# Optimization experiments

Measured on AMD Instinct MI355X. Metric: run time of the kernel, lower is better.

The kernel has to match this reference:

```python
import jax, jax.numpy as jnp
import numpy as np

B, T, DM, H, D = 2, 2048, 1024, 16, 64
SCALE = D ** -0.5


def setup_inputs() -> dict:
    key = jax.random.key(0)
    ks = jax.random.split(key, 7)
    std = DM ** -0.5
    inp = {
        "x": jax.random.normal(ks[0], (B, T, DM), dtype=jnp.float32),
        "Wq_re": jax.random.normal(ks[1], (DM, H * D), dtype=jnp.float32) * std,
        "Wq_im": jax.random.normal(ks[2], (DM, H * D), dtype=jnp.float32) * std,
        "Wk_re": jax.random.normal(ks[3], (DM, H * D), dtype=jnp.float32) * std,
        "Wk_im": jax.random.normal(ks[4], (DM, H * D), dtype=jnp.float32) * std,
        "Wv": jax.random.normal(ks[5], (DM, H * D), dtype=jnp.float32) * std,
        "Wo": jax.random.normal(ks[6], (H * D, DM), dtype=jnp.float32) * std,
    }
    # standard RoPE angle cache: theta[t, d] = t * 10000^(-d/D)
    inv_freq = 1.0 / (10000.0 ** (np.arange(D, dtype=np.float32) / D))
    ang = np.arange(T, dtype=np.float32)[:, None] * inv_freq[None, :]
    inp["cos"] = jnp.asarray(np.cos(ang))
    inp["sin"] = jnp.asarray(np.sin(ang))
    return inp


def _split(x, W):
    # [B,T,DM] @ [DM,H*D] -> [B,H,T,D]
    return (x @ W).reshape(B, T, H, D).transpose(0, 2, 1, 3)


def reference(x, Wq_re, Wq_im, Wk_re, Wk_im, Wv, Wo, cos, sin):
    q_re, q_im = _split(x, Wq_re), _split(x, Wq_im)
    k_re, k_im = _split(x, Wk_re), _split(x, Wk_im)

    # complex RoPE: rotate (re, im) by e^{i*theta}; cos/sin broadcast over b,h
    c = cos[None, None]  # [1,1,T,D]
    s = sin[None, None]
    q_re, q_im = q_re * c - q_im * s, q_re * s + q_im * c
    k_re, k_im = k_re * c - k_im * s, k_re * s + k_im * c

    # Hermitian inner product real part: q_re.k_re + q_im.k_im
    scores = (jnp.einsum("bhqd,bhkd->bhqk", q_re, k_re)
              + jnp.einsum("bhqd,bhkd->bhqk", q_im, k_im)) * SCALE

    causal = jnp.tril(jnp.ones((T, T), dtype=bool))
    scores = jnp.where(causal[None, None], scores, -jnp.inf)
    weights = jax.nn.softmax(scores, axis=-1)

    v = _split(x, Wv)
    out = jnp.einsum("bhqk,bhkd->bhqd", weights, v)  # [B,H,T,D]
    out = out.transpose(0, 2, 1, 3).reshape(B, T, H * D)
    return out @ Wo
```

## Files before the change

kernel.cpp:

```cpp
#include <hip/hip_runtime.h>
#include <math.h>

#define SCALE_ 0.125f

typedef _Float16 half_t;
typedef __attribute__((ext_vector_type(8))) _Float16 f16x8;
typedef __attribute__((ext_vector_type(4))) _Float16 f16x4;
typedef __attribute__((ext_vector_type(4))) float f32x4;

#define AS1 __attribute__((address_space(1)))
#define AS3 __attribute__((address_space(3)))

__device__ __forceinline__ f32x4 mfma16(f16x8 a, f16x8 b, f32x4 c) {
  return __builtin_amdgcn_mfma_f32_16x16x32_f16(a, b, c, 0, 0, 0);
}
__device__ __forceinline__ void gload16(const void* g, void* l) {
  __builtin_amdgcn_global_load_lds((const AS1 void*)g, (AS3 void*)l, 16, 0, 0);
}
__device__ __forceinline__ void split2(float f, half_t* h, half_t* l) {
  half_t hh = (half_t)f;
  *h = hh;
  *l = (half_t)(f - (float)hh);
}

__global__ __launch_bounds__(256) void convw_kernel(
    const float* __restrict__ W0, const float* __restrict__ W1,
    const float* __restrict__ W2, const float* __restrict__ W3,
    const float* __restrict__ W4, const float* __restrict__ W5,
    half_t* __restrict__ wh, half_t* __restrict__ wl)
{
  const int z = blockIdx.z;
  const float* W = (z == 0) ? W0 : (z == 1) ? W1 : (z == 2) ? W2
                  : (z == 3) ? W3 : (z == 4) ? W4 : W5;
  half_t* outh = wh + z * 1048576;
  half_t* outl = wl + z * 1048576;
  const int n0 = blockIdx.x * 32, k0 = blockIdx.y * 32;
  const int t = threadIdx.x, r = t >> 3, c4 = (t & 7) * 4;
  __shared__ float lds[32][33];
  float4 v = *(const float4*)&W[(k0 + r) * 1024 + n0 + c4];
  lds[r][c4 + 0] = v.x; lds[r][c4 + 1] = v.y;
  lds[r][c4 + 2] = v.z; lds[r][c4 + 3] = v.w;
  __syncthreads();
  f16x4 oh, ol;
#pragma unroll
  for (int j = 0; j < 4; ++j) {
    const float f = lds[c4 + j][r];
    half_t hv, lv; split2(f, &hv, &lv);
    oh[j] = hv; ol[j] = lv;
  }
  *(f16x4*)&outh[(n0 + r) * 1024 + k0 + c4] = oh;
  *(f16x4*)&outl[(n0 + r) * 1024 + k0 + c4] = ol;
}

__global__ __launch_bounds__(256) void convx_kernel(
    const float* __restrict__ x, half_t* __restrict__ xh, half_t* __restrict__ xl)
{
  const int i = (blockIdx.x * 256 + threadIdx.x) * 4;
  float4 v = *(const float4*)&x[i];
  float vv[4] = {v.x, v.y, v.z, v.w};
  f16x4 oh, ol;
#pragma unroll
  for (int j = 0; j < 4; ++j) {
    half_t hv, lv; split2(vv[j], &hv, &lv);
    oh[j] = hv; ol[j] = lv;
  }
  *(f16x4*)&xh[i] = oh;
  *(f16x4*)&xl[i] = ol;
}

__global__ __launch_bounds__(256) void gemm_kernel(
    const half_t* __restrict__ Agh, const half_t* __restrict__ Agl,
    const half_t* __restrict__ wh, const half_t* __restrict__ wl,
    half_t* __restrict__ qth, half_t* __restrict__ qtl,
    half_t* __restrict__ kth, half_t* __restrict__ ktl,
    half_t* __restrict__ vTh, half_t* __restrict__ vTl,
    float* __restrict__ outp, int final_mode)
{
  __shared__ half_t Ash[4096], Asl[4096], Bsh[4096], Bsl[4096];
  const int z = blockIdx.z;
  const int widx = final_mode ? 5 : z;
  const half_t* Bth = wh + widx * 1048576;
  const half_t* Btl = wl + widx * 1048576;

  const int n0 = blockIdx.x * 128, m0 = blockIdx.y * 128;
  const int tid = threadIdx.x, lane = tid & 63, wid = tid >> 6;
  const int wr = wid >> 1, wc = wid & 1, l15 = lane & 15, l4 = lane >> 4;

  f32x4 acc[4][4];
#pragma unroll
  for (int i = 0; i < 4; ++i)
#pragma unroll
    for (int j = 0; j < 4; ++j) acc[i][j] = (f32x4){0.f, 0.f, 0.f, 0.f};

  const int s0 = wid * 64 + lane, s1 = s0 + 256;
  const int r0 = s0 >> 2, c0 = (s0 & 3) * 8;
  const int r1 = s1 >> 2, c1 = (s1 & 3) * 8;
  half_t* Ah0 = Ash + wid * 512;        half_t* Ah1 = Ash + 2048 + wid * 512;
  half_t* Al0 = Asl + wid * 512;        half_t* Al1 = Asl + 2048 + wid * 512;
  half_t* Bh0 = Bsh + wid * 512;        half_t* Bh1 = Bsh + 2048 + wid * 512;
  half_t* Bl0 = Bsl + wid * 512;        half_t* Bl1 = Bsl + 2048 + wid * 512;

  for (int k0 = 0; k0 < 1024; k0 += 32) {
    __syncthreads();
    gload16(Agh + (m0 + r0) * 1024 + k0 + c0, Ah0);
    gload16(Agh + (m0 + r1) * 1024 + k0 + c1, Ah1);
    gload16(Agl + (m0 + r0) * 1024 + k0 + c0, Al0);
    gload16(Agl + (m0 + r1) * 1024 + k0 + c1, Al1);
    gload16(Bth + (n0 + r0) * 1024 + k0 + c0, Bh0);
    gload16(Bth + (n0 + r1) * 1024 + k0 + c1, Bh1);
    gload16(Btl + (n0 + r0) * 1024 + k0 + c0, Bl0);
    gload16(Btl + (n0 + r1) * 1024 + k0 + c1, Bl1);
    __syncthreads();
    f16x8 ah[4], al[4], bh[4], bl[4];
#pragma unroll
    for (int i = 0; i < 4; ++i) {
      const int ro = (wr * 64 + i * 16 + l15) * 32 + l4 * 8;
      ah[i] = *(const f16x8*)&Ash[ro];
      al[i] = *(const f16x8*)&Asl[ro];
    }
#pragma unroll
    for (int j = 0; j < 4; ++j) {
      const int ro = (wc * 64 + j * 16 + l15) * 32 + l4 * 8;
      bh[j] = *(const f16x8*)&Bsh[ro];
      bl[j] = *(const f16x8*)&Bsl[ro];
    }
#pragma unroll
    for (int i = 0; i < 4; ++i)
#pragma unroll
      for (int j = 0; j < 4; ++j) {
        acc[i][j] = mfma16(ah[i], bh[j], acc[i][j]);
        acc[i][j] = mfma16(ah[i], bl[j], acc[i][j]);
        acc[i][j] = mfma16(al[i], bh[j], acc[i][j]);
      }
  }

#pragma unroll
  for (int i = 0; i < 4; ++i) {
    const int mb = m0 + wr * 64 + i * 16 + l4 * 4;
#pragma unroll
    for (int j = 0; j < 4; ++j) {
      const int n = n0 + wc * 64 + j * 16 + l15;
      if (final_mode) {
#pragma unroll
        for (int r = 0; r < 4; ++r) outp[(mb + r) * 1024 + n] = acc[i][j][r];
      } else if (z < 4) {
        half_t* dh = (z < 2) ? qth : kth;
        half_t* dl = (z < 2) ? qtl : ktl;
        const int colr = (n >> 6) * 128 + (n & 63) + ((z & 1) ? 64 : 0);
#pragma unroll
        for (int r = 0; r < 4; ++r) {
          half_t hv, lv; split2(acc[i][j][r], &hv, &lv);
          dh[(mb + r) * 2048 + colr] = hv;
          dl[(mb + r) * 2048 + colr] = lv;
        }
      } else {
        const int hh = n >> 6, d = n & 63;
        const int bq = mb >> 11, t = mb & 2047;
        f16x4 vh4, vl4;
#pragma unroll
        for (int r = 0; r < 4; ++r) {
          half_t hv, lv; split2(acc[i][j][r], &hv, &lv);
          vh4[r] = hv; vl4[r] = lv;
        }
        const int off = ((bq * 16 + hh) * 64 + d) * 2048 + t;
        *(f16x4*)&vTh[off] = vh4;
        *(f16x4*)&vTl[off] = vl4;
      }
    }
  }
}

__global__ __launch_bounds__(256) void rope_kernel(
    const half_t* __restrict__ qth, const half_t* __restrict__ qtl,
    const half_t* __restrict__ kth, const half_t* __restrict__ ktl,
    const float* __restrict__ cosb, const float* __restrict__ sinb,
    half_t* __restrict__ qbh, half_t* __restrict__ qbl,
    half_t* __restrict__ kbh, half_t* __restrict__ kbl)
{
  const int z = blockIdx.y;
  const int g = blockIdx.x * 4 + (threadIdx.x >> 6);
  const int d = threadIdx.x & 63;
  const int m = g >> 4, h = g & 15;
  const int b = m >> 11, t = m & 2047;
  const half_t* sh = (z ? kth : qth) + m * 2048 + h * 128;
  const half_t* sl = (z ? ktl : qtl) + m * 2048 + h * 128;
  const float re = (float)sh[d] + (float)sl[d];
  const float im = (float)sh[64 + d] + (float)sl[64 + d];
  const float c = cosb[t * 64 + d], s = sinb[t * 64 + d];
  float rer = re * c - im * s;
  float imr = re * s + im * c;
  if (z == 0) { rer *= SCALE_; imr *= SCALE_; }
  half_t* dh = (z ? kbh : qbh) + ((b * 16 + h) * 2048 + t) * 128;
  half_t* dl = (z ? kbl : qbl) + ((b * 16 + h) * 2048 + t) * 128;
  half_t hv, lv;
  split2(rer, &hv, &lv); dh[d] = hv;      dl[d] = lv;
  split2(imr, &hv, &lv); dh[64 + d] = hv; dl[64 + d] = lv;
}

__global__ __launch_bounds__(256) void attn_kernel(
    const half_t* __restrict__ qbh, const half_t* __restrict__ qbl,
    const half_t* __restrict__ kbh, const half_t* __restrict__ kbl,
    const half_t* __restrict__ vTh, const half_t* __restrict__ vTl,
    half_t* __restrict__ abh, half_t* __restrict__ abl)
{
  const int qt = (int)gridDim.x - 1 - (int)blockIdx.x;
  const int bh = blockIdx.y;
  const int b = bh >> 4, h = bh & 15;
  const int tid = threadIdx.x, lane = tid & 63, w = tid >> 6;
  const int l15 = lane & 15, l4 = lane >> 4;
  const int q0 = qt * 64;

  __shared__ half_t Kh[8192], Kl[8192];
  __shared__ half_t Vh[4096], Vl[4096];
  __shared__ half_t Ph[4096], Pl[4096];

  f16x8 qh[4], ql[4];
  {
    const int qoff = (bh * 2048 + q0 + w * 16 + l15) * 128;
#pragma unroll
    for (int c = 0; c < 4; ++c) {
      qh[c] = *(const f16x8*)(qbh + qoff + c * 32 + l4 * 8);
      ql[c] = *(const f16x8*)(qbl + qoff + c * 32 + l4 * 8);
    }
  }

  f32x4 o[4];
#pragma unroll
  for (int n = 0; n < 4; ++n) o[n] = (f32x4){0.f, 0.f, 0.f, 0.f};
  float mrow[4] = {-3e38f, -3e38f, -3e38f, -3e38f};
  float lrow[4] = {0.f, 0.f, 0.f, 0.f};

  const half_t* kh_p = kbh + bh * 2048 * 128;
  const half_t* kl_p = kbl + bh * 2048 * 128;
  const half_t* vh_p = vTh + bh * 64 * 2048;
  const half_t* vl_p = vTl + bh * 64 * 2048;

  for (int kt = 0; kt <= qt; ++kt) {
    const int k0 = kt * 64;
    __syncthreads();
    {
      f16x8 kh_[4], kl_[4], vh_[2], vl_[2];
#pragma unroll
      for (int it = 0; it < 4; ++it) {
        const int sIdx = it * 256 + tid, row = sIdx >> 4, slot = sIdx & 15;
        kh_[it] = *(const f16x8*)(kh_p + (k0 + row) * 128 + slot * 8);
        kl_[it] = *(const f16x8*)(kl_p + (k0 + row) * 128 + slot * 8);
      }
#pragma unroll
      for (int it = 0; it < 2; ++it) {
        const int sIdx = it * 256 + tid, row = sIdx >> 3, slot = sIdx & 7;
        vh_[it] = *(const f16x8*)(vh_p + row * 2048 + k0 + slot * 8);
        vl_[it] = *(const f16x8*)(vl_p + row * 2048 + k0 + slot * 8);
      }
#pragma unroll
      for (int it = 0; it < 4; ++it) {
        const int sIdx = it * 256 + tid, row = sIdx >> 4, slot = sIdx & 15;
        const int sp = (slot & 8) | ((slot & 7) ^ (row & 7));
        *(f16x8*)&Kh[row * 128 + sp * 8] = kh_[it];
        *(f16x8*)&Kl[row * 128 + sp * 8] = kl_[it];
      }
#pragma unroll
      for (int it = 0; it < 2; ++it) {
        const int sIdx = it * 256 + tid, row = sIdx >> 3, slot = sIdx & 7;
        const int sp = slot ^ (row & 7);
        *(f16x8*)&Vh[row * 64 + sp * 8] = vh_[it];
        *(f16x8*)&Vl[row * 64 + sp * 8] = vl_[it];
      }
    }
    __syncthreads();

    f32x4 s[4];
#pragma unroll
    for (int n = 0; n < 4; ++n) s[n] = (f32x4){0.f, 0.f, 0.f, 0.f};
#pragma unroll
    for (int c = 0; c < 4; ++c) {
#pragma unroll
      for (int n = 0; n < 4; ++n) {
        const int row = n * 16 + l15;
        const int slot = c * 4 + l4;
        const int sp = (slot & 8) | ((slot & 7) ^ (row & 7));
        const f16x8 kfh = *(const f16x8*)&Kh[row * 128 + sp * 8];
        const f16x8 kfl = *(const f16x8*)&Kl[row * 128 + sp * 8];
        s[n] = mfma16(qh[c], kfh, s[n]);
        s[n] = mfma16(qh[c], kfl, s[n]);
        s[n] = mfma16(ql[c], kfh, s[n]);
      }
    }

    if (kt == qt) {
#pragma unroll
      for (int n = 0; n < 4; ++n)
#pragma unroll
        for (int r = 0; r < 4; ++r)
          if (n * 16 + l15 > w * 16 + l4 * 4 + r) s[n][r] = -3e38f;
    }

#pragma unroll
    for (int r = 0; r < 4; ++r) {
      float mx = fmaxf(fmaxf(s[0][r], s[1][r]), fmaxf(s[2][r], s[3][r]));
      mx = fmaxf(mx, __shfl_xor(mx, 1));
      mx = fmaxf(mx, __shfl_xor(mx, 2));
      mx = fmaxf(mx, __shfl_xor(mx, 4));
      mx = fmaxf(mx, __shfl_xor(mx, 8));
      const float mnew = fmaxf(mrow[r], mx);
      const float alpha = __expf(mrow[r] - mnew);
      float p[4];
#pragma unroll
      for (int n = 0; n < 4; ++n) p[n] = __expf(s[n][r] - mnew);
      float rs = p[0] + p[1] + p[2] + p[3];
      rs += __shfl_xor(rs, 1);
      rs += __shfl_xor(rs, 2);
      rs += __shfl_xor(rs, 4);
      rs += __shfl_xor(rs, 8);
      lrow[r] = lrow[r] * alpha + rs;
      mrow[r] = mnew;
#pragma unroll
      for (int n = 0; n < 4; ++n) o[n][r] *= alpha;
      const int prow = w * 16 + l4 * 4 + r;
#pragma unroll
      for (int n = 0; n < 4; ++n) {
        const int col = n * 16 + l15;
        const int sp = (col >> 3) ^ (prow & 7);
        half_t hv, lv; split2(p[n], &hv, &lv);
        Ph[prow * 64 + sp * 8 + (col & 7)] = hv;
        Pl[prow * 64 + sp * 8 + (col & 7)] = lv;
      }
    }
    __syncthreads();

#pragma unroll
    for (int c = 0; c < 2; ++c) {
      const int prow = w * 16 + l15;
      const int sp = (c * 4 + l4) ^ (prow & 7);
      const f16x8 pfh = *(const f16x8*)&Ph[prow * 64 + sp * 8];
      const f16x8 pfl = *(const f16x8*)&Pl[prow * 64 + sp * 8];
#pragma unroll
      for (int n = 0; n < 4; ++n) {
        const int vrow = n * 16 + l15;
        const int sp2 = (c * 4 + l4) ^ (vrow & 7);
        const f16x8 vfh = *(const f16x8*)&Vh[vrow * 64 + sp2 * 8];
        const f16x8 vfl = *(const f16x8*)&Vl[vrow * 64 + sp2 * 8];
        o[n] = mfma16(pfh, vfh, o[n]);
        o[n] = mfma16(pfh, vfl, o[n]);
        o[n] = mfma16(pfl, vfh, o[n]);
      }
    }
  }

  const int mg = b * 2048 + q0 + w * 16 + l4 * 4;
#pragma unroll
  for (int r = 0; r < 4; ++r) {
    const float inv = 1.0f / lrow[r];
    const int m = mg + r;
#pragma unroll
    for (int n = 0; n < 4; ++n) {
      half_t hv, lv; split2(o[n][r] * inv, &hv, &lv);
      abh[m * 1024 + h * 64 + n * 16 + l15] = hv;
      abl[m * 1024 + h * 64 + n * 16 + l15] = lv;
    }
  }
}

extern "C" void kernel_launch(void* const* d_in, const int* in_sizes, int n_in,
                              void* d_out, int out_size, void* d_ws,
                              size_t ws_size, hipStream_t stream) {
  const float* x    = (const float*)d_in[0];
  const float* Wqre = (const float*)d_in[1];
  const float* Wqim = (const float*)d_in[2];
  const float* Wkre = (const float*)d_in[3];
  const float* Wkim = (const float*)d_in[4];
  const float* Wv   = (const float*)d_in[5];
  const float* Wo   = (const float*)d_in[6];
  const float* cosb = (const float*)d_in[7];
  const float* sinb = (const float*)d_in[8];

  char* w = (char*)d_ws;
  const size_t MB = (size_t)1 << 20;
  half_t* wh6 = (half_t*)(w + 0 * MB);
  half_t* wl6 = (half_t*)(w + 12 * MB);
  half_t* xh  = (half_t*)(w + 24 * MB);
  half_t* xl  = (half_t*)(w + 32 * MB);
  half_t* qth = (half_t*)(w + 40 * MB);
  half_t* qtl = (half_t*)(w + 56 * MB);
  half_t* kth = (half_t*)(w + 72 * MB);
  half_t* ktl = (half_t*)(w + 88 * MB);
  half_t* qbh = (half_t*)(w + 104 * MB);
  half_t* qbl = (half_t*)(w + 120 * MB);
  half_t* kbh = (half_t*)(w + 136 * MB);
  half_t* kbl = (half_t*)(w + 152 * MB);
  half_t* vTh = (half_t*)(w + 168 * MB);
  half_t* vTl = (half_t*)(w + 176 * MB);
  half_t* abh = (half_t*)(w + 40 * MB);
  half_t* abl = (half_t*)(w + 48 * MB);

  dim3 blk(256);
  convw_kernel<<<dim3(32, 32, 6), blk, 0, stream>>>(Wqre, Wqim, Wkre, Wkim, Wv,
                                                    Wo, wh6, wl6);
  convx_kernel<<<dim3(4096), blk, 0, stream>>>(x, xh, xl);
  gemm_kernel<<<dim3(8, 32, 5), blk, 0, stream>>>(xh, xl, wh6, wl6, qth, qtl,
                                                  kth, ktl, vTh, vTl, nullptr, 0);
  rope_kernel<<<dim3(16384, 2), blk, 0, stream>>>(qth, qtl, kth, ktl, cosb,
                                                  sinb, qbh, qbl, kbh, kbl);
  attn_kernel<<<dim3(32, 32), blk, 0, stream>>>(qbh, qbl, kbh, kbl, vTh, vTl,
                                                abh, abl);
  gemm_kernel<<<dim3(8, 32, 1), blk, 0, stream>>>(abh, abl, wh6, wl6, nullptr,
                                                  nullptr, nullptr, nullptr,
                                                  nullptr, nullptr,
                                                  (float*)d_out, 1);
}
```

Before: 565.9 us.

## Restructure attention kernel: 512-thread blocks, 32-key double-buffered async LDS loads

The attention kernel now uses 512 threads (8 waves) per block covering 128 query rows, with 32-key tiles. K/V tiles are loaded with global_load_lds into double-buffered shared memory so the next tile's load overlaps compute. Waves whose queries lie entirely before a tile skip its compute, and the P tile is written and read within a wave without a block barrier. This aims to hide global latency and cut register-staged copies and barriers, at the cost of smaller MFMA tiles per iteration and more loop iterations.

Result: no change. 570.6 us (+0.8%).

```diff
diff --git a/kernel.cpp b/kernel.cpp
--- a/kernel.cpp
+++ b/kernel.cpp
@@ -197,7 +197,7 @@
   split2(imr, &hv, &lv); dh[64 + d] = hv; dl[64 + d] = lv;
 }
 
-__global__ __launch_bounds__(256) void attn_kernel(
+__global__ __launch_bounds__(512) void attn_kernel(
     const half_t* __restrict__ qbh, const half_t* __restrict__ qbl,
     const half_t* __restrict__ kbh, const half_t* __restrict__ kbl,
     const half_t* __restrict__ vTh, const half_t* __restrict__ vTl,
@@ -208,10 +208,10 @@
   const int b = bh >> 4, h = bh & 15;
   const int tid = threadIdx.x, lane = tid & 63, w = tid >> 6;
   const int l15 = lane & 15, l4 = lane >> 4;
-  const int q0 = qt * 64;
-
-  __shared__ half_t Kh[8192], Kl[8192];
-  __shared__ half_t Vh[4096], Vl[4096];
+  const int q0 = qt * 128;
+
+  __shared__ half_t Kh[2][4096], Kl[2][4096];
+  __shared__ half_t Vh[2][2048], Vl[2][2048];
   __shared__ half_t Ph[4096], Pl[4096];
 
   f16x8 qh[4], ql[4];
@@ -230,84 +230,81 @@
   float mrow[4] = {-3e38f, -3e38f, -3e38f, -3e38f};
   float lrow[4] = {0.f, 0.f, 0.f, 0.f};
 
-  const half_t* kh_p = kbh + bh * 2048 * 128;
-  const half_t* kl_p = kbl + bh * 2048 * 128;
-  const half_t* vh_p = vTh + bh * 64 * 2048;
-  const half_t* vl_p = vTl + bh * 64 * 2048;
-
-  for (int kt = 0; kt <= qt; ++kt) {
-    const int k0 = kt * 64;
+  const half_t* kh_p = kbh + (size_t)bh * 2048 * 128;
+  const half_t* kl_p = kbl + (size_t)bh * 2048 * 128;
+  const half_t* vh_p = vTh + (size_t)bh * 64 * 2048;
+  const half_t* vl_p = vTl + (size_t)bh * 64 * 2048;
+
+  const int krow = w * 4 + (lane >> 4);
+  const int ks = lane & 15;
+  const int kg = (ks & 8) | ((ks & 7) ^ (krow & 7));
+  const int vrow = (w & 3) * 16 + (lane >> 2);
+  const int vs = lane & 3;
+  const int vg = vs ^ ((vrow >> 1) & 3);
+  const bool vhi = (w < 4);
+
+  const int nkt = 4 * (qt + 1);
+  const int qminw = q0 + w * 16, qmaxw = qminw + 15;
+
+  gload16(kh_p + (krow) * 128 + kg * 8, &Kh[0][w * 512]);
+  gload16(kl_p + (krow) * 128 + kg * 8, &Kl[0][w * 512]);
+  if (vhi) gload16(vh_p + vrow * 2048 + vg * 8, &Vh[0][(w & 3) * 512]);
+  else     gload16(vl_p + vrow * 2048 + vg * 8, &Vl[0][(w & 3) * 512]);
+
+  for (int kt = 0; kt < nkt; ++kt) {
+    const int k0 = kt * 32;
+    const int cb = kt & 1;
     __syncthreads();
+
     {
-      f16x8 kh_[4], kl_[4], vh_[2], vl_[2];
-#pragma unroll
-      for (int it = 0; it < 4; ++it) {
-        const int sIdx = it * 256 + tid, row = sIdx >> 4, slot = sIdx & 15;
-        kh_[it] = *(const f16x8*)(kh_p + (k0 + row) * 128 + slot * 8);
-        kl_[it] = *(const f16x8*)(kl_p + (k0 + row) * 128 + slot * 8);
-      }
-#pragma unroll
-      for (int it = 0; it < 2; ++it) {
-        const int sIdx = it * 256 + tid, row = sIdx >> 3, slot = sIdx & 7;
-        vh_[it] = *(const f16x8*)(vh_p + row * 2048 + k0 + slot * 8);
-        vl_[it] = *(const f16x8*)(vl_p + row * 2048 + k0 + slot * 8);
-      }
-#pragma unroll
-      for (int it = 0; it < 4; ++it) {
-        const int sIdx = it * 256 + tid, row = sIdx >> 4, slot = sIdx & 15;
-        const int sp = (slot & 8) | ((slot & 7) ^ (row & 7));
-        *(f16x8*)&Kh[row * 128 + sp * 8] = kh_[it];
-        *(f16x8*)&Kl[row * 128 + sp * 8] = kl_[it];
-      }
-#pragma unroll
-      for (int it = 0; it < 2; ++it) {
-        const int sIdx = it * 256 + tid, row = sIdx >> 3, slot = sIdx & 7;
-        const int sp = slot ^ (row & 7);
-        *(f16x8*)&Vh[row * 64 + sp * 8] = vh_[it];
-        *(f16x8*)&Vl[row * 64 + sp * 8] = vl_[it];
-      }
-    }
-    __syncthreads();
-
-    f32x4 s[4];
-#pragma unroll
-    for (int n = 0; n < 4; ++n) s[n] = (f32x4){0.f, 0.f, 0.f, 0.f};
+      const int k0n = (kt + 1 < nkt) ? k0 + 32 : 0;
+      const int nb = cb ^ 1;
+      gload16(kh_p + (k0n + krow) * 128 + kg * 8, &Kh[nb][w * 512]);
+      gload16(kl_p + (k0n + krow) * 128 + kg * 8, &Kl[nb][w * 512]);
+      if (vhi) gload16(vh_p + vrow * 2048 + k0n + vg * 8, &Vh[nb][(w & 3) * 512]);
+      else     gload16(vl_p + vrow * 2048 + k0n + vg * 8, &Vl[nb][(w & 3) * 512]);
+    }
+
+    if (k0 > qmaxw) continue;
+
+    f32x4 s[2];
+    s[0] = (f32x4){0.f, 0.f, 0.f, 0.f};
+    s[1] = (f32x4){0.f, 0.f, 0.f, 0.f};
 #pragma unroll
     for (int c = 0; c < 4; ++c) {
 #pragma unroll
-      for (int n = 0; n < 4; ++n) {
+      for (int n = 0; n < 2; ++n) {
         const int row = n * 16 + l15;
-        const int slot = c * 4 + l4;
-        const int sp = (slot & 8) | ((slot & 7) ^ (row & 7));
-        const f16x8 kfh = *(const f16x8*)&Kh[row * 128 + sp * 8];
-        const f16x8 kfl = *(const f16x8*)&Kl[row * 128 + sp * 8];
+        const int co = c * 4 + l4;
+        const int sr = (co & 8) | ((co & 7) ^ (row & 7));
+        const f16x8 kfh = *(const f16x8*)&Kh[cb][row * 128 + sr * 8];
+        const f16x8 kfl = *(const f16x8*)&Kl[cb][row * 128 + sr * 8];
         s[n] = mfma16(qh[c], kfh, s[n]);
         s[n] = mfma16(qh[c], kfl, s[n]);
         s[n] = mfma16(ql[c], kfh, s[n]);
       }
     }
 
-    if (kt == qt) {
-#pragma unroll
-      for (int n = 0; n < 4; ++n)
+    if (k0 + 31 > qminw) {
+#pragma unroll
+      for (int n = 0; n < 2; ++n)
 #pragma unroll
         for (int r = 0; r < 4; ++r)
-          if (n * 16 + l15 > w * 16 + l4 * 4 + r) s[n][r] = -3e38f;
+          if (k0 + n * 16 + l15 > qminw + l4 * 4 + r) s[n][r] = -3e38f;
     }
 
 #pragma unroll
     for (int r = 0; r < 4; ++r) {
-      float mx = fmaxf(fmaxf(s[0][r], s[1][r]), fmaxf(s[2][r], s[3][r]));
+      float mx = fmaxf(s[0][r], s[1][r]);
       mx = fmaxf(mx, __shfl_xor(mx, 1));
       mx = fmaxf(mx, __shfl_xor(mx, 2));
       mx = fmaxf(mx, __shfl_xor(mx, 4));
       mx = fmaxf(mx, __shfl_xor(mx, 8));
       const float mnew = fmaxf(mrow[r], mx);
       const float alpha = __expf(mrow[r] - mnew);
-      float p[4];
-#pragma unroll
-      for (int n = 0; n < 4; ++n) p[n] = __expf(s[n][r] - mnew);
-      float rs = p[0] + p[1] + p[2] + p[3];
+      const float p0 = __expf(s[0][r] - mnew);
+      const float p1 = __expf(s[1][r] - mnew);
+      float rs = p0 + p1;
       rs += __shfl_xor(rs, 1);
       rs += __shfl_xor(rs, 2);
       rs += __shfl_xor(rs, 4);
@@ -317,29 +314,33 @@
 #pragma unroll
       for (int n = 0; n < 4; ++n) o[n][r] *= alpha;
       const int prow = w * 16 + l4 * 4 + r;
+      const int psw = (prow >> 2) & 3;
+      half_t hv, lv;
+      split2(p0, &hv, &lv);
+      {
+        const int col = l15, sp = (col >> 3) ^ psw;
+        Ph[prow * 32 + sp * 8 + (col & 7)] = hv;
+        Pl[prow * 32 + sp * 8 + (col & 7)] = lv;
+      }
+      split2(p1, &hv, &lv);
+      {
+        const int col = 16 + l15, sp = (col >> 3) ^ psw;
+        Ph[prow * 32 + sp * 8 + (col & 7)] = hv;
+        Pl[prow * 32 + sp * 8 + (col & 7)] = lv;
+      }
+    }
+
+    {
+      const int prow = w * 16 + l15;
+      const int spp = l4 ^ ((prow >> 2) & 3);
+      const f16x8 pfh = *(const f16x8*)&Ph[prow * 32 + spp * 8];
+      const f16x8 pfl = *(const f16x8*)&Pl[prow * 32 + spp * 8];
 #pragma unroll
       for (int n = 0; n < 4; ++n) {
-        const int col = n * 16 + l15;
-        const int sp = (col >> 3) ^ (prow & 7);
-        half_t hv, lv; split2(p[n], &hv, &lv);
-        Ph[prow * 64 + sp * 8 + (col & 7)] = hv;
-        Pl[prow * 64 + sp * 8 + (col & 7)] = lv;
-      }
-    }
-    __syncthreads();
-
-#pragma unroll
-    for (int c = 0; c < 2; ++c) {
-      const int prow = w * 16 + l15;
-      const int sp = (c * 4 + l4) ^ (prow & 7);
-      const f16x8 pfh = *(const f16x8*)&Ph[prow * 64 + sp * 8];
-      const f16x8 pfl = *(const f16x8*)&Pl[prow * 64 + sp * 8];
-#pragma unroll
-      for (int n = 0; n < 4; ++n) {
-        const int vrow = n * 16 + l15;
-        const int sp2 = (c * 4 + l4) ^ (vrow & 7);
-        const f16x8 vfh = *(const f16x8*)&Vh[vrow * 64 + sp2 * 8];
-        const f16x8 vfl = *(const f16x8*)&Vl[vrow * 64 + sp2 * 8];
+        const int vr = n * 16 + l15;
+        const int sv = l4 ^ ((vr >> 1) & 3);
+        const f16x8 vfh = *(const f16x8*)&Vh[cb][vr * 32 + sv * 8];
+        const f16x8 vfl = *(const f16x8*)&Vl[cb][vr * 32 + sv * 8];
         o[n] = mfma16(pfh, vfh, o[n]);
         o[n] = mfma16(pfh, vfl, o[n]);
         o[n] = mfma16(pfl, vfh, o[n]);
@@ -401,8 +402,8 @@
                                                   kth, ktl, vTh, vTl, nullptr, 0);
   rope_kernel<<<dim3(16384, 2), blk, 0, stream>>>(qth, qtl, kth, ktl, cosb,
                                                   sinb, qbh, qbl, kbh, kbl);
-  attn_kernel<<<dim3(32, 32), blk, 0, stream>>>(qbh, qbl, kbh, kbl, vTh, vTl,
-                                                abh, abl);
+  attn_kernel<<<dim3(16, 32), dim3(512), 0, stream>>>(qbh, qbl, kbh, kbl, vTh,
+                                                      vTl, abh, abl);
   gemm_kernel<<<dim3(8, 32, 1), blk, 0, stream>>>(abh, abl, wh6, wl6, nullptr,
                                                   nullptr, nullptr, nullptr,
                                                   nullptr, nullptr,
```
